# Optimization experiments

Measured on AMD Instinct MI355X. Metric: run time of the kernel, lower is better.

## Reference

```python
import jax, jax.numpy as jnp
import numpy as np

N_NODES = 4096
N_EDGES = 16384
D_IN = 128
HID = 1024


def _linear_params(key, fan_in, fan_out):
    kw, kb = jax.random.split(key)
    bound = 1.0 / np.sqrt(fan_in)
    W = jax.random.uniform(kw, (fan_in, fan_out), jnp.float32, -bound, bound)
    b = jax.random.uniform(kb, (fan_out,), jnp.float32, -bound, bound)
    return W, b


def setup_inputs() -> dict:
    key = jax.random.key(0)
    ks = jax.random.split(key, 10)
    H = jax.random.normal(ks[0], (N_NODES, D_IN), jnp.float32)
    e = jax.random.uniform(ks[1], (N_NODES,), jnp.float32)
    # true incidence matrices: one-hot source/destination node per edge
    src = jax.random.randint(ks[2], (N_EDGES,), 0, N_NODES)
    dst = jax.random.randint(ks[3], (N_EDGES,), 0, N_NODES)
    Ro = jax.nn.one_hot(src, N_NODES, dtype=jnp.float32)  # [E, N]
    Ri = jax.nn.one_hot(dst, N_NODES, dtype=jnp.float32)  # [E, N]
    W1, b1 = _linear_params(ks[4], 3 * D_IN, HID)
    W2, b2 = _linear_params(ks[5], HID, HID)
    W3, b3 = _linear_params(ks[6], HID, HID // 2)
    W4, b4 = _linear_params(ks[7], HID // 2, HID // 4)
    W5, b5 = _linear_params(ks[8], HID // 4, 1)
    return {"H": H, "Ro": Ro, "Ri": Ri, "e": e,
            "W1": W1, "b1": b1, "W2": W2, "b2": b2, "W3": W3, "b3": b3,
            "W4": W4, "b4": b4, "W5": W5, "b5": b5}


def reference(H, Ro, Ri, e, W1, b1, W2, b2, W3, b3, W4, b4, W5, b5):
    eH = e[:, None] * H                      # [N, D]
    Ho = Ri.T @ (Ro @ eH)                    # aggregate over edges -> [N, D]
    Hi = Ro.T @ (Ri @ eH)                    # [N, D]
    x = jnp.concatenate([Ho, H, Hi], axis=1)  # [N, 3D]
    x = jnp.tanh(x @ W1 + b1)
    x = jnp.tanh(x @ W2 + b2)
    x = jnp.tanh(x @ W3 + b3)
    x = jnp.tanh(x @ W4 + b4)
    return jax.nn.sigmoid(x @ W5 + b5)       # [N, 1]
```

## Files before the change

kernel.cpp:

```cpp
#include <hip/hip_runtime.h>
#include <hip/hip_bf16.h>
#include <math.h>

#define N_NODES 4096
#define N_EDGES 16384
#define D_IN 128
#define HID 1024

typedef short s8v __attribute__((ext_vector_type(8)));
typedef float f4v __attribute__((ext_vector_type(4)));

__device__ __forceinline__ unsigned short f2b(float v) {
    union { float f; unsigned int u; } c; c.f = v;
    unsigned int u = c.u + 0x7fffu + ((c.u >> 16) & 1u);
    return (unsigned short)(u >> 16);
}
__device__ __forceinline__ void glds16(const unsigned short* g, unsigned short* l) {
    __builtin_amdgcn_global_load_lds(
        (const __attribute__((address_space(1))) void*)g,
        (__attribute__((address_space(3))) void*)l, 16, 0, 0);
}

__global__ void extract_scatter_wt(const float* __restrict__ Ro, const float* __restrict__ Ri,
                                   const float* __restrict__ H, const float* __restrict__ e,
                                   float* __restrict__ xf,
                                   const float* __restrict__ W1, unsigned short* __restrict__ wt1,
                                   const float* __restrict__ W2, unsigned short* __restrict__ wt2,
                                   const float* __restrict__ W3, unsigned short* __restrict__ wt3,
                                   const float* __restrict__ W4, unsigned short* __restrict__ wt4) {
    int b = blockIdx.x, t = threadIdx.x;
    if (b < 4096) {
        int edge = (b * 256 + t) >> 6;
        int l = t & 63;
        const f4v* ro4 = (const f4v*)(Ro + (size_t)edge * N_NODES);
        const f4v* ri4 = (const f4v*)(Ri + (size_t)edge * N_NODES);
        int src = -1, dst = -1;
        for (int g = 0; g < 4; ++g) {
            f4v va[4], vb[4];
            bool needA = (src < 0), needB = (dst < 0);
            if (needA) {
#pragma unroll
                for (int i = 0; i < 4; ++i)
                    va[i] = __builtin_nontemporal_load(&ro4[(g * 4 + i) * 64 + l]);
            }
            if (needB) {
#pragma unroll
                for (int i = 0; i < 4; ++i)
                    vb[i] = __builtin_nontemporal_load(&ri4[(g * 4 + i) * 64 + l]);
            }
            if (needA) {
#pragma unroll
                for (int i = 0; i < 4; ++i) {
                    if (src < 0) {
                        f4v v = va[i];
                        bool hit = (v.x != 0.0f) | (v.y != 0.0f) | (v.z != 0.0f) | (v.w != 0.0f);
                        unsigned long long m = __ballot(hit);
                        if (m) {
                            int fl = __ffsll((long long)m) - 1;
                            int idx = 0;
                            if (hit) idx = ((g * 4 + i) * 64 + l) * 4 +
                                           (v.x != 0.0f ? 0 : v.y != 0.0f ? 1 : v.z != 0.0f ? 2 : 3);
                            src = __shfl(idx, fl);
                        }
                    }
                }
            }
            if (needB) {
#pragma unroll
                for (int i = 0; i < 4; ++i) {
                    if (dst < 0) {
                        f4v v = vb[i];
                        bool hit = (v.x != 0.0f) | (v.y != 0.0f) | (v.z != 0.0f) | (v.w != 0.0f);
                        unsigned long long m = __ballot(hit);
                        if (m) {
                            int fl = __ffsll((long long)m) - 1;
                            int idx = 0;
                            if (hit) idx = ((g * 4 + i) * 64 + l) * 4 +
                                           (v.x != 0.0f ? 0 : v.y != 0.0f ? 1 : v.z != 0.0f ? 2 : 3);
                            dst = __shfl(idx, fl);
                        }
                    }
                }
            }
            if (src >= 0 && dst >= 0) break;
        }
        float es = e[src], ed = e[dst];
        if (l < 32) {
            int f = l * 4;
            float4 h = *(const float4*)(H + (size_t)src * 128 + f);
            float* o = xf + (size_t)dst * 256 + f;
            atomicAdd(o + 0, es * h.x); atomicAdd(o + 1, es * h.y);
            atomicAdd(o + 2, es * h.z); atomicAdd(o + 3, es * h.w);
        } else {
            int f = (l - 32) * 4;
            float4 h = *(const float4*)(H + (size_t)dst * 128 + f);
            float* o = xf + (size_t)src * 256 + 128 + f;
            atomicAdd(o + 0, ed * h.x); atomicAdd(o + 1, ed * h.y);
            atomicAdd(o + 2, ed * h.z); atomicAdd(o + 3, ed * h.w);
        }
        return;
    }
    int wb = b - 4096;
    const float* W; unsigned short* WT; int K, N, tb;
    if (wb < 384)       { W = W1; WT = wt1; K = 384;  N = 1024; tb = wb; }
    else if (wb < 1408) { W = W2; WT = wt2; K = 1024; N = 1024; tb = wb - 384; }
    else if (wb < 1920) { W = W3; WT = wt3; K = 1024; N = 512;  tb = wb - 1408; }
    else                { W = W4; WT = wt4; K = 512;  N = 256;  tb = wb - 1920; }
    __shared__ float tile[32][33];
    int ntx = N >> 5;
    int tk = tb / ntx, tn = tb - tk * ntx;
    int tr = t >> 5, tc = t & 31;
#pragma unroll
    for (int i = 0; i < 4; ++i)
        tile[tr + i * 8][tc] = W[(size_t)(tk * 32 + tr + i * 8) * N + tn * 32 + tc];
    __syncthreads();
#pragma unroll
    for (int i = 0; i < 4; ++i)
        WT[(size_t)(tn * 32 + tr + i * 8) * K + tk * 32 + tc] = f2b(tile[tc][tr + i * 8]);
}

__global__ __launch_bounds__(256)
void build_a1(const float* __restrict__ xf, const float* __restrict__ H,
              unsigned short* __restrict__ A1) {
    int gid = blockIdx.x * 256 + threadIdx.x;
    int row = gid / 48;
    int g = gid - row * 48;
    const float* sp;
    if (g < 16)      sp = xf + (size_t)row * 256 + g * 8;
    else if (g < 32) sp = H  + (size_t)row * 128 + (g - 16) * 8;
    else             sp = xf + (size_t)row * 256 + 128 + (g - 32) * 8;
    float4 f0 = *(const float4*)sp, f1 = *(const float4*)(sp + 4);
    s8v pk;
    pk[0] = (short)f2b(f0.x); pk[1] = (short)f2b(f0.y);
    pk[2] = (short)f2b(f0.z); pk[3] = (short)f2b(f0.w);
    pk[4] = (short)f2b(f1.x); pk[5] = (short)f2b(f1.y);
    pk[6] = (short)f2b(f1.z); pk[7] = (short)f2b(f1.w);
    *(s8v*)&A1[(size_t)row * 384 + g * 8] = pk;
}

template<int BM, int BN>
__global__ __launch_bounds__(256)
void gemm_tanh(const unsigned short* __restrict__ A, const unsigned short* __restrict__ BT,
               const float* __restrict__ bias, unsigned short* __restrict__ C,
               int M, int N, int K) {
    constexpr int BK = 32;
    constexpr int MI = BM / 32, NI = BN / 32;
    constexpr int AITER = BM / 64, BITER = BN / 64;
    __shared__ unsigned short As[BM * BK];
    __shared__ unsigned short Bs[BN * BK];
    int t = threadIdx.x;
    int l = t & 63, w = t >> 6;
    int wm = w >> 1, wn = w & 1;
    int q = l >> 4, r16 = l & 15;
    int m0 = blockIdx.y * BM, n0 = blockIdx.x * BN;

    f4v acc[MI][NI] = {};

    for (int k0 = 0; k0 < K; k0 += BK) {
        __syncthreads();
#pragma unroll
        for (int i = 0; i < AITER; ++i) {
            int c = (i * 4 + w) * 64 + l;
            int row = c >> 2, ko = (c & 3) * 8;
            glds16(&A[(size_t)(m0 + row) * K + k0 + ko], &As[c * 8]);
        }
#pragma unroll
        for (int i = 0; i < BITER; ++i) {
            int c = (i * 4 + w) * 64 + l;
            int row = c >> 2, ko = (c & 3) * 8;
            glds16(&BT[(size_t)(n0 + row) * K + k0 + ko], &Bs[c * 8]);
        }
        __syncthreads();
        s8v a[MI], b[NI];
#pragma unroll
        for (int mi = 0; mi < MI; ++mi)
            a[mi] = *(const s8v*)&As[(wm * (BM / 2) + mi * 16 + r16) * BK + q * 8];
#pragma unroll
        for (int ni = 0; ni < NI; ++ni)
            b[ni] = *(const s8v*)&Bs[(wn * (BN / 2) + ni * 16 + r16) * BK + q * 8];
#pragma unroll
        for (int mi = 0; mi < MI; ++mi)
#pragma unroll
            for (int ni = 0; ni < NI; ++ni)
                acc[mi][ni] = __builtin_amdgcn_mfma_f32_16x16x32_bf16(a[mi], b[ni], acc[mi][ni], 0, 0, 0);
    }
#pragma unroll
    for (int mi = 0; mi < MI; ++mi)
#pragma unroll
        for (int ni = 0; ni < NI; ++ni) {
            int col = n0 + wn * (BN / 2) + ni * 16 + r16;
            float bv = bias[col];
#pragma unroll
            for (int r = 0; r < 4; ++r) {
                int row = m0 + wm * (BM / 2) + mi * 16 + q * 4 + r;
                C[(size_t)row * N + col] = f2b(tanhf(acc[mi][ni][r] + bv));
            }
        }
}

__global__ __launch_bounds__(256)
void gemm45(const unsigned short* __restrict__ A, const unsigned short* __restrict__ BT,
            const float* __restrict__ b4, const float* __restrict__ W5,
            const float* __restrict__ b5, float* __restrict__ out) {
    constexpr int BK = 32, K = 512, NN = 256;
    constexpr int NI = 8;
    __shared__ unsigned short As[32 * BK];
    __shared__ unsigned short Bs[NN * BK];
    __shared__ float part[32][2];
    int t = threadIdx.x;
    int l = t & 63, w = t >> 6;
    int wm = w >> 1, wn = w & 1;
    int q = l >> 4, r16 = l & 15;
    int m0 = blockIdx.y * 32;

    f4v acc[NI] = {};

    for (int k0 = 0; k0 < K; k0 += BK) {
        __syncthreads();
        if (w < 2) {
            int c = w * 64 + l;
            int row = c >> 2, ko = (c & 3) * 8;
            glds16(&A[(size_t)(m0 + row) * K + k0 + ko], &As[c * 8]);
        }
#pragma unroll
        for (int i = 0; i < 4; ++i) {
            int c = (i * 4 + w) * 64 + l;
            int row = c >> 2, ko = (c & 3) * 8;
            glds16(&BT[(size_t)row * K + k0 + ko], &Bs[c * 8]);
        }
        __syncthreads();
        s8v a = *(const s8v*)&As[(wm * 16 + r16) * BK + q * 8];
        s8v b[NI];
#pragma unroll
        for (int ni = 0; ni < NI; ++ni)
            b[ni] = *(const s8v*)&Bs[(wn * 128 + ni * 16 + r16) * BK + q * 8];
#pragma unroll
        for (int ni = 0; ni < NI; ++ni)
            acc[ni] = __builtin_amdgcn_mfma_f32_16x16x32_bf16(a, b[ni], acc[ni], 0, 0, 0);
    }

    float partial[4] = {0.f, 0.f, 0.f, 0.f};
#pragma unroll
    for (int ni = 0; ni < NI; ++ni) {
        int col = wn * 128 + ni * 16 + r16;
        float bv = b4[col], wv = W5[col];
#pragma unroll
        for (int r = 0; r < 4; ++r)
            partial[r] += tanhf(acc[ni][r] + bv) * wv;
    }
#pragma unroll
    for (int off = 1; off < 16; off <<= 1)
#pragma unroll
        for (int r = 0; r < 4; ++r)
            partial[r] += __shfl_xor(partial[r], off);
    if (r16 == 0)
#pragma unroll
        for (int r = 0; r < 4; ++r)
            part[wm * 16 + q * 4 + r][wn] = partial[r];
    __syncthreads();
    if (t < 32) {
        float s = part[t][0] + part[t][1] + b5[0];
        out[m0 + t] = 1.0f / (1.0f + expf(-s));
    }
}

extern "C" void kernel_launch(void* const* d_in, const int* in_sizes, int n_in,
                              void* d_out, int out_size, void* d_ws, size_t ws_size,
                              hipStream_t stream) {
    const float* H  = (const float*)d_in[0];
    const float* Ro = (const float*)d_in[1];
    const float* Ri = (const float*)d_in[2];
    const float* e  = (const float*)d_in[3];
    const float* W1 = (const float*)d_in[4];  const float* b1 = (const float*)d_in[5];
    const float* W2 = (const float*)d_in[6];  const float* b2 = (const float*)d_in[7];
    const float* W3 = (const float*)d_in[8];  const float* b3 = (const float*)d_in[9];
    const float* W4 = (const float*)d_in[10]; const float* b4 = (const float*)d_in[11];
    const float* W5 = (const float*)d_in[12]; const float* b5 = (const float*)d_in[13];
    float* out = (float*)d_out;

    char* p = (char*)d_ws;
    auto alloc = [&](size_t bytes) -> void* {
        void* r = (void*)p;
        p += (bytes + 255) & ~(size_t)255;
        return r;
    };
    float* xf = (float*)alloc((size_t)N_NODES * 256 * 4);
    unsigned short* a1  = (unsigned short*)alloc((size_t)N_NODES * 384 * 2);
    unsigned short* h1  = (unsigned short*)alloc((size_t)N_NODES * HID * 2);
    unsigned short* h2  = (unsigned short*)alloc((size_t)N_NODES * HID * 2);
    unsigned short* h3  = (unsigned short*)alloc((size_t)N_NODES * (HID / 2) * 2);
    unsigned short* wt1 = (unsigned short*)alloc((size_t)HID * 384 * 2);
    unsigned short* wt2 = (unsigned short*)alloc((size_t)HID * HID * 2);
    unsigned short* wt3 = (unsigned short*)alloc((size_t)(HID / 2) * HID * 2);
    unsigned short* wt4 = (unsigned short*)alloc((size_t)(HID / 4) * (HID / 2) * 2);

    extract_scatter_wt<<<4096 + 2048, 256, 0, stream>>>(Ro, Ri, H, e, xf,
                                                        W1, wt1, W2, wt2, W3, wt3, W4, wt4);

    build_a1<<<(N_NODES * 48) / 256, 256, 0, stream>>>(xf, H, a1);

    gemm_tanh<128, 64><<<dim3(HID / 64, N_NODES / 128), 256, 0, stream>>>(a1, wt1, b1, h1, N_NODES, HID, 384);
    gemm_tanh<128, 64><<<dim3(HID / 64, N_NODES / 128), 256, 0, stream>>>(h1, wt2, b2, h2, N_NODES, HID, HID);
    gemm_tanh<64, 64><<<dim3((HID / 2) / 64, N_NODES / 64), 256, 0, stream>>>(h2, wt3, b3, h3, N_NODES, HID / 2, HID);

    gemm45<<<dim3(1, N_NODES / 32), 256, 0, stream>>>(h3, wt4, b4, W5, b5, out);
}
```

Before: 564.2 us.

## Replace atomic scatter aggregation with CSR-style gather via counting sort

Instead of scattering e-weighted H rows into an fp32 buffer with per-element float atomics and then converting it to bf16, the edge extraction now records src/dst indices and per-node degree counts. A single-block scan builds offsets, a fill pass builds per-node incoming and outgoing edge lists, and a gather kernel sums neighbor rows and writes bf16 A1 directly. This removes float atomic contention and the separate build pass, at the cost of four extra small kernel launches, a serial one-block scan, and a gather kernel using 64-thread blocks.

New measurement: 562.7 us. About the same (-0.3%).

```diff
diff --git a/kernel.cpp b/kernel.cpp
--- a/kernel.cpp
+++ b/kernel.cpp
@@ -21,13 +21,17 @@
         (__attribute__((address_space(3))) void*)l, 16, 0, 0);
 }
 
-__global__ void extract_scatter_wt(const float* __restrict__ Ro, const float* __restrict__ Ri,
-                                   const float* __restrict__ H, const float* __restrict__ e,
-                                   float* __restrict__ xf,
-                                   const float* __restrict__ W1, unsigned short* __restrict__ wt1,
-                                   const float* __restrict__ W2, unsigned short* __restrict__ wt2,
-                                   const float* __restrict__ W3, unsigned short* __restrict__ wt3,
-                                   const float* __restrict__ W4, unsigned short* __restrict__ wt4) {
+__global__ void zero_counts(int* __restrict__ c) {
+    c[blockIdx.x * 256 + threadIdx.x] = 0;
+}
+
+__global__ void extract_wt(const float* __restrict__ Ro, const float* __restrict__ Ri,
+                           int* __restrict__ src_arr, int* __restrict__ dst_arr,
+                           int* __restrict__ counts,
+                           const float* __restrict__ W1, unsigned short* __restrict__ wt1,
+                           const float* __restrict__ W2, unsigned short* __restrict__ wt2,
+                           const float* __restrict__ W3, unsigned short* __restrict__ wt3,
+                           const float* __restrict__ W4, unsigned short* __restrict__ wt4) {
     int b = blockIdx.x, t = threadIdx.x;
     if (b < 4096) {
         int edge = (b * 256 + t) >> 6;
@@ -84,19 +88,11 @@
             }
             if (src >= 0 && dst >= 0) break;
         }
-        float es = e[src], ed = e[dst];
-        if (l < 32) {
-            int f = l * 4;
-            float4 h = *(const float4*)(H + (size_t)src * 128 + f);
-            float* o = xf + (size_t)dst * 256 + f;
-            atomicAdd(o + 0, es * h.x); atomicAdd(o + 1, es * h.y);
-            atomicAdd(o + 2, es * h.z); atomicAdd(o + 3, es * h.w);
-        } else {
-            int f = (l - 32) * 4;
-            float4 h = *(const float4*)(H + (size_t)dst * 128 + f);
-            float* o = xf + (size_t)src * 256 + 128 + f;
-            atomicAdd(o + 0, ed * h.x); atomicAdd(o + 1, ed * h.y);
-            atomicAdd(o + 2, ed * h.z); atomicAdd(o + 3, ed * h.w);
+        if (l == 0) {
+            src_arr[edge] = src;
+            dst_arr[edge] = dst;
+            atomicAdd(&counts[dst], 1);
+            atomicAdd(&counts[4096 + src], 1);
         }
         return;
     }
@@ -119,23 +115,77 @@
         WT[(size_t)(tn * 32 + tr + i * 8) * K + tk * 32 + tc] = f2b(tile[tc][tr + i * 8]);
 }
 
-__global__ __launch_bounds__(256)
-void build_a1(const float* __restrict__ xf, const float* __restrict__ H,
-              unsigned short* __restrict__ A1) {
-    int gid = blockIdx.x * 256 + threadIdx.x;
-    int row = gid / 48;
-    int g = gid - row * 48;
-    const float* sp;
-    if (g < 16)      sp = xf + (size_t)row * 256 + g * 8;
-    else if (g < 32) sp = H  + (size_t)row * 128 + (g - 16) * 8;
-    else             sp = xf + (size_t)row * 256 + 128 + (g - 32) * 8;
-    float4 f0 = *(const float4*)sp, f1 = *(const float4*)(sp + 4);
-    s8v pk;
-    pk[0] = (short)f2b(f0.x); pk[1] = (short)f2b(f0.y);
-    pk[2] = (short)f2b(f0.z); pk[3] = (short)f2b(f0.w);
-    pk[4] = (short)f2b(f1.x); pk[5] = (short)f2b(f1.y);
-    pk[6] = (short)f2b(f1.z); pk[7] = (short)f2b(f1.w);
-    *(s8v*)&A1[(size_t)row * 384 + g * 8] = pk;
+__global__ __launch_bounds__(1024)
+void scan_offsets(const int* __restrict__ counts, int* __restrict__ starts,
+                  int* __restrict__ cursors) {
+    __shared__ int part[1024];
+    int t = threadIdx.x;
+    for (int a = 0; a < 2; ++a) {
+        const int* c = counts + a * 4096;
+        int v[4], s = 0;
+#pragma unroll
+        for (int i = 0; i < 4; ++i) { v[i] = c[t * 4 + i]; s += v[i]; }
+        part[t] = s;
+        __syncthreads();
+        for (int off = 1; off < 1024; off <<= 1) {
+            int x = (t >= off) ? part[t - off] : 0;
+            __syncthreads();
+            part[t] += x;
+            __syncthreads();
+        }
+        int o = part[t] - s;
+#pragma unroll
+        for (int i = 0; i < 4; ++i) {
+            starts[a * 4096 + t * 4 + i]  = o;
+            cursors[a * 4096 + t * 4 + i] = o;
+            o += v[i];
+        }
+        __syncthreads();
+    }
+}
+
+__global__ void fill_lists(const int* __restrict__ src_arr, const int* __restrict__ dst_arr,
+                           int* __restrict__ cursors,
+                           int* __restrict__ in_list, int* __restrict__ out_list) {
+    int e = blockIdx.x * 256 + threadIdx.x;
+    int s = src_arr[e], d = dst_arr[e];
+    int p = atomicAdd(&cursors[d], 1);
+    in_list[p] = e;
+    int p2 = atomicAdd(&cursors[4096 + s], 1);
+    out_list[p2] = e;
+}
+
+__global__ __launch_bounds__(64)
+void gather_a1(const float* __restrict__ H, const float* __restrict__ e_arr,
+               const int* __restrict__ src_arr, const int* __restrict__ dst_arr,
+               const int* __restrict__ starts, const int* __restrict__ counts,
+               const int* __restrict__ in_list, const int* __restrict__ out_list,
+               unsigned short* __restrict__ A1) {
+    int n = blockIdx.x;
+    int l = threadIdx.x;
+    bool lo = l < 32;
+    int f = (lo ? l : l - 32) * 4;
+    int base = lo ? starts[n] : starts[4096 + n];
+    int cnt  = lo ? counts[n] : counts[4096 + n];
+    const int* list  = lo ? in_list : out_list;
+    const int* other = lo ? src_arr : dst_arr;
+    f4v acc = {0.f, 0.f, 0.f, 0.f};
+    for (int i = 0; i < cnt; ++i) {
+        int eidx = list[base + i];
+        int node = other[eidx];
+        float s = e_arr[node];
+        f4v h = *(const f4v*)(H + (size_t)node * 128 + f);
+        acc.x += s * h.x; acc.y += s * h.y; acc.z += s * h.z; acc.w += s * h.w;
+    }
+    ushort4 pk;
+    pk.x = f2b(acc.x); pk.y = f2b(acc.y); pk.z = f2b(acc.z); pk.w = f2b(acc.w);
+    *(ushort4*)&A1[(size_t)n * 384 + (lo ? 0 : 256) + f] = pk;
+    if (lo) {
+        f4v h = *(const f4v*)(H + (size_t)n * 128 + f);
+        ushort4 ph;
+        ph.x = f2b(h.x); ph.y = f2b(h.y); ph.z = f2b(h.z); ph.w = f2b(h.w);
+        *(ushort4*)&A1[(size_t)n * 384 + 128 + f] = ph;
+    }
 }
 
 template<int BM, int BN>
@@ -284,7 +334,13 @@
         p += (bytes + 255) & ~(size_t)255;
         return r;
     };
-    float* xf = (float*)alloc((size_t)N_NODES * 256 * 4);
+    int* counts   = (int*)alloc(8192 * 4);
+    int* starts   = (int*)alloc(8192 * 4);
+    int* cursors  = (int*)alloc(8192 * 4);
+    int* src_arr  = (int*)alloc(N_EDGES * 4);
+    int* dst_arr  = (int*)alloc(N_EDGES * 4);
+    int* in_list  = (int*)alloc(N_EDGES * 4);
+    int* out_list = (int*)alloc(N_EDGES * 4);
     unsigned short* a1  = (unsigned short*)alloc((size_t)N_NODES * 384 * 2);
     unsigned short* h1  = (unsigned short*)alloc((size_t)N_NODES * HID * 2);
     unsigned short* h2  = (unsigned short*)alloc((size_t)N_NODES * HID * 2);
@@ -294,10 +350,17 @@
     unsigned short* wt3 = (unsigned short*)alloc((size_t)(HID / 2) * HID * 2);
     unsigned short* wt4 = (unsigned short*)alloc((size_t)(HID / 4) * (HID / 2) * 2);
 
-    extract_scatter_wt<<<4096 + 2048, 256, 0, stream>>>(Ro, Ri, H, e, xf,
-                                                        W1, wt1, W2, wt2, W3, wt3, W4, wt4);
-
-    build_a1<<<(N_NODES * 48) / 256, 256, 0, stream>>>(xf, H, a1);
+    zero_counts<<<32, 256, 0, stream>>>(counts);
+
+    extract_wt<<<4096 + 2048, 256, 0, stream>>>(Ro, Ri, src_arr, dst_arr, counts,
+                                                W1, wt1, W2, wt2, W3, wt3, W4, wt4);
+
+    scan_offsets<<<1, 1024, 0, stream>>>(counts, starts, cursors);
+
+    fill_lists<<<64, 256, 0, stream>>>(src_arr, dst_arr, cursors, in_list, out_list);
+
+    gather_a1<<<N_NODES, 64, 0, stream>>>(H, e, src_arr, dst_arr, starts, counts,
+                                          in_list, out_list, a1);
 
     gemm_tanh<128, 64><<<dim3(HID / 64, N_NODES / 128), 256, 0, stream>>>(a1, wt1, b1, h1, N_NODES, HID, 384);
     gemm_tanh<128, 64><<<dim3(HID / 64, N_NODES / 128), 256, 0, stream>>>(h1, wt2, b2, h2, N_NODES, HID, HID);
```
